# Performance work log

Hardware: AMD Instinct MI355X
Metric: run time of the kernel (lower is better)

The kernel has to match this reference:

```python
import jax, jax.numpy as jnp
import numpy as np
import math

H, N, L_DEFAULT = 1024, 64, 2048
DT_MIN, DT_MAX = 0.001, 0.1
EPS = 1e-7


def hippo_skew_evals(n):
    # eigenvalues of (Hippo - Hippo.T)/2, sorted by descending imaginary part
    i = np.arange(n, dtype=np.float64)
    x = 2.0 * i + 1.0
    hippo = np.sqrt(np.outer(x, x)) * np.tri(n, n, -1)  # strictly lower triangular
    skew = (hippo - hippo.T) / 2.0
    evals = np.linalg.eigvals(skew)
    return evals[np.argsort(-evals.imag)]


def setup_inputs() -> dict:
    rng = np.random.default_rng(0)
    # Lambda init: hippo_skew_pos_imag -> w = evals(2N)[:N] - 0.5 (real part -0.5 < 0)
    w = hippo_skew_evals(2 * N)[:N] - 0.5
    Lambda_log_neg_re = np.log(-w.real).astype(np.float32)  # (N,)
    Lambda_im = w.imag.astype(np.float32)                   # (N,)
    # log_dt ~ U[log dt_min, log dt_max], tiled to (H,2) since sep_dt_re_im=True
    log_dt = (math.log(DT_MIN) + rng.random(H) * (math.log(DT_MAX) - math.log(DT_MIN))).astype(np.float32)
    log_dt = np.tile(log_dt[:, None], (1, 2))               # (H,2)
    W = rng.standard_normal((H, N, 2)).astype(np.float32)   # real view of complex (H,N)
    return {
        'log_dt': jnp.asarray(log_dt),
        'Lambda_log_neg_re': jnp.asarray(Lambda_log_neg_re),
        'Lambda_im': jnpp if False else jnp.asarray(Lambda_im),
        'W': jnp.asarray(W),
        'L': L_DEFAULT,
    }


def _reciprocal_clamped(x, eps=EPS):
    # conj(x) / max(|x|^2, eps^2)  -- matches DSS reciprocal(..., clamp=True)
    norm_sq = jnp.maximum((x * jnp.conj(x)).real, eps * eps)
    return jnp.conj(x) / norm_sq


def reference(log_dt, Lambda_log_neg_re, Lambda_im, W, L):
    Lam = -jnp.exp(Lambda_log_neg_re) + 1j * Lambda_im              # (N,) complex
    Wc = W[..., 0] + 1j * W[..., 1]                                 # (H,N) complex
    dt = jnp.exp(log_dt)                                            # (H,2)
    # sep_dt_re_im: separate step sizes for real and imaginary parts
    dt_Lambda = dt[:, 0:1] * Lam.real + 1j * (dt[:, 1:2] * Lam.imag)  # (H,N) complex
    pos = jnp.arange(L, dtype=log_dt.dtype)                          # (L,)
    S = jnp.exp(dt_Lambda[None, :, :] * pos[:, None, None])          # (L,H,N) complex
    Wk = Wc * (jnp.exp(dt_Lambda) - 1.0) * _reciprocal_clamped(Lam)  # (H,N)
    # kernel: real part of sum_n W[h,n] * S[l,h,n]
    return jnp.einsum('hn,lhn->lh', Wk, S).real.astype(jnp.float32)  # (L,H)
```

## Files before the change

kernel.cpp:

```cpp
#include <hip/hip_runtime.h>
#include <math.h>

#define H_DIM 1024
#define N_DIM 64

typedef __attribute__((ext_vector_type(8))) _Float16 f16x8;
typedef __attribute__((ext_vector_type(4))) float f32x4;

__device__ __forceinline__ float2 cmul(float2 a, float2 b) {
    return make_float2(fmaf(a.x, b.x, -(a.y * b.y)),
                       fmaf(a.x, b.y,   a.y * b.x));
}

__device__ __forceinline__ unsigned pkh(float x, float y) {
    union { _Float16 h[2]; unsigned u; } p;
    p.h[0] = (_Float16)x; p.h[1] = (_Float16)y;
    return p.u;
}


__global__ __launch_bounds__(256, 4) void dss_mfma2(
    const float* __restrict__ log_dt,
    const float* __restrict__ llnr,
    const float* __restrict__ limv,
    const float* __restrict__ W,
    const int*   __restrict__ Lp,
    float* __restrict__ out)
{
    __shared__ unsigned lds_raw[4 * 2 * 16 * 68];

    const int tid  = threadIdx.x;
    const int w    = tid >> 6;
    const int lane = tid & 63;

    int htile, g;
    if (gridDim.y == 8 && gridDim.x == 128) {
        const int id = blockIdx.x + (blockIdx.y << 7);
        g = id & 7;
        const int q = id >> 3;
        htile = 4 * (q & 31) + (q >> 5);
    } else { htile = blockIdx.x; g = blockIdx.y; }

    const int h0 = htile * 8;
    const int L  = *Lp;
    const int fr = lane & 15;
    const int kg = lane >> 4;

    const float lre = -__expf(llnr[lane]);
    const float lmi = limv[lane];
    const float den = fmaxf(fmaf(lre, lre, lmi * lmi), 1e-14f);
    const float rde = __builtin_amdgcn_rcpf(den);
    const float rr = lre * rde, ri = -lmi * rde;

    unsigned* Atab = lds_raw + w * (2 * 16 * 68);
    unsigned* Btab = Atab + 16 * 68;

    f32x4 accs[2];

    #pragma unroll
    for (int j = 0; j < 2; ++j) {
        const int h = h0 + 2 * w + j;
        const float dt0 = __expf(log_dt[2 * h]);
        const float dt1 = __expf(log_dt[2 * h + 1]);
        const float a = dt0 * lre;
        const float b = dt1 * lmi;
        const float eA = __expf(a);
        const float sb = __sinf(b), cbv = __cosf(b);
        const float2 s = make_float2(eA * cbv, eA * sb);

        const float2 wc = ((const float2*)W)[(size_t)h * N_DIM + lane];
        const float2 em1 = make_float2(s.x - 1.0f, s.y);
        const float2 t  = make_float2(em1.x * rr - em1.y * ri,
                                      em1.x * ri + em1.y * rr);
        const float2 wk = make_float2(wc.x * t.x - wc.y * t.y,
                                      wc.x * t.y + wc.y * t.x);

        const float2 s2 = cmul(s, s), s4 = cmul(s2, s2), s8 = cmul(s4, s4);
        const float2 s12 = cmul(s8, s4), s16 = cmul(s8, s8);
        const float2 s32 = cmul(s16, s16), s64 = cmul(s32, s32);
        const float2 s128 = cmul(s64, s64), s192 = cmul(s128, s64);
        const float2 s256 = cmul(s128, s128);
        const float2 s512 = cmul(s256, s256), s1024 = cmul(s512, s512);

        float2 w0 = wk;
        if (g & 1) w0 = cmul(w0, s256);
        if (g & 2) w0 = cmul(w0, s512);
        if (g & 4) w0 = cmul(w0, s1024);

        float2 Bv[16];
        Bv[0] = make_float2(1.0f, 0.0f); Bv[4] = s4; Bv[8] = s8; Bv[12] = s12;
        #pragma unroll
        for (int k = 1; k < 4; ++k) {
            Bv[k]      = cmul(Bv[k - 1], s);
            Bv[4 + k]  = cmul(Bv[4 + k - 1], s);
            Bv[8 + k]  = cmul(Bv[8 + k - 1], s);
            Bv[12 + k] = cmul(Bv[12 + k - 1], s);
        }
        float2 Av[16];
        Av[0] = w0; Av[4] = cmul(w0, s64); Av[8] = cmul(w0, s128); Av[12] = cmul(w0, s192);
        #pragma unroll
        for (int k = 1; k < 4; ++k) {
            Av[k]      = cmul(Av[k - 1], s16);
            Av[4 + k]  = cmul(Av[4 + k - 1], s16);
            Av[8 + k]  = cmul(Av[8 + k - 1], s16);
            Av[12 + k] = cmul(Av[12 + k - 1], s16);
        }

        #pragma unroll
        for (int q = 0; q < 16; ++q)
            Atab[q * 68 + lane] = pkh(Av[q].x, Av[q].y);
        #pragma unroll
        for (int r = 0; r < 16; ++r)
            Btab[r * 68 + lane] = pkh(Bv[r].x, -Bv[r].y);

        f32x4 acc = {0.0f, 0.0f, 0.0f, 0.0f};
        #pragma unroll
        for (int c = 0; c < 4; ++c) {
            const f16x8 af = *(const f16x8*)&Atab[fr * 68 + 16 * c + 4 * kg];
            const f16x8 bf = *(const f16x8*)&Btab[fr * 68 + 16 * c + 4 * kg];
            acc = __builtin_amdgcn_mfma_f32_16x16x32_f16(af, bf, acc, 0, 0, 0);
        }
        accs[j] = acc;
    }

    __syncthreads();
    float* scr = (float*)lds_raw;
    #pragma unroll
    for (int j = 0; j < 2; ++j) {
        const int hl = 2 * w + j;
        #pragma unroll
        for (int reg = 0; reg < 4; ++reg)
            scr[(64 * kg + 16 * reg + fr) * 12 + hl] = accs[j][reg];
    }
    __syncthreads();

    const float4* scr4 = (const float4*)scr;
    float4* out4 = (float4*)out;
    const int l0 = g * 256;
    #pragma unroll
    for (int i = 0; i < 2; ++i) {
        const int flat = i * 256 + tid;
        const int l = flat >> 1, q = flat & 1;
        const int gl = l0 + l;
        if (gl < L)
            out4[(size_t)gl * (H_DIM / 4) + htile * 2 + q] = scr4[l * 3 + q];
    }
}


#define HT 64
#define CHUNK 16

__global__ __launch_bounds__(256) void dss_kernel_fb(
    const float* __restrict__ log_dt,
    const float* __restrict__ lam_log_neg_re,
    const float* __restrict__ lam_im,
    const float* __restrict__ W,
    const int*   __restrict__ Lp,
    float* __restrict__ out,
    int H, int N)
{
    __shared__ float4 params[N_DIM * HT];
    const int tid = threadIdx.x;
    const int h0 = blockIdx.x * HT;
    const int l0_blk = blockIdx.y * 64;
    const int L = *Lp;
    const float2* __restrict__ W2 = (const float2*)W;

    for (int flat = tid; flat < N * HT; flat += 256) {
        const int hl = flat & (HT - 1);
        const int n  = flat >> 6;
        const int h  = h0 + hl;
        const float dt0 = expf(log_dt[2 * h]);
        const float dt1 = expf(log_dt[2 * h + 1]);
        const float lre = -expf(lam_log_neg_re[n]);
        const float lmi = lam_im[n];
        const float a = dt0 * lre;
        const float b = dt1 * lmi;
        const float eA = expf(a);
        float sb, cb;
        sincosf(b, &sb, &cb);
        const float em1r = eA * cb - 1.0f;
        const float em1i = eA * sb;
        const float den = fmaxf(lre * lre + lmi * lmi, 1e-14f);
        const float rr =  lre / den;
        const float ri = -lmi / den;
        const float2 wc = W2[h * N + n];
        const float trm = em1r * rr - em1i * ri;
        const float tim = em1r * ri + em1i * rr;
        params[flat] = make_float4(a, b,
                                   wc.x * trm - wc.y * tim,
                                   wc.x * tim + wc.y * trm);
    }
    __syncthreads();

    const int hl = tid & (HT - 1);
    const int chunk = tid >> 6;
    const int l0 = l0_blk + chunk * CHUNK;
    if (l0 >= L) return;

    float acc[CHUNK];
    #pragma unroll
    for (int k = 0; k < CHUNK; ++k) acc[k] = 0.0f;

    const double TWO_PI  = 6.283185307179586476925286766559;
    const double INV_2PI = 0.15915494309189533576888376337251;

    for (int n = 0; n < N; ++n) {
        const float4 pp = params[n * HT + hl];
        const float a = pp.x, b = pp.y, wr = pp.z, wi = pp.w;
        double ph = (double)b * (double)l0;
        ph -= TWO_PI * rint(ph * INV_2PI);
        const float th = (float)ph;
        const float e0 = expf(a * (float)l0);
        float s0, c0;
        sincosf(th, &s0, &c0);
        float zr = e0 * c0;
        float zi = e0 * s0;
        const float eA = expf(a);
        float sb, cb;
        sincosf(b, &sb, &cb);
        const float str = eA * cb;
        const float sti = eA * sb;
        #pragma unroll
        for (int k = 0; k < CHUNK; ++k) {
            acc[k] = fmaf(wr, zr, fmaf(-wi, zi, acc[k]));
            const float nzr = zr * str - zi * sti;
            const float nzi = fmaf(zr, sti, zi * str);
            zr = nzr; zi = nzi;
        }
    }

    #pragma unroll
    for (int k = 0; k < CHUNK; ++k) {
        const int l = l0 + k;
        if (l < L) out[(size_t)l * H + h0 + hl] = acc[k];
    }
}


extern "C" void kernel_launch(void* const* d_in, const int* in_sizes, int n_in,
                              void* d_out, int out_size, void* d_ws, size_t ws_size,
                              hipStream_t stream) {
    const float* log_dt = (const float*)d_in[0];
    const float* llnr   = (const float*)d_in[1];
    const float* lim    = (const float*)d_in[2];
    const float* W      = (const float*)d_in[3];
    const int*   Lp     = (const int*)d_in[4];

    const int H = in_sizes[0] / 2;
    const int N = in_sizes[1];
    const int L = out_size / (H > 0 ? H : 1);

    if (H == H_DIM && N == N_DIM && L <= 2048) {
        dim3 grid(H_DIM / 8, (L + 255) / 256);
        dss_mfma2<<<grid, 256, 0, stream>>>(log_dt, llnr, lim, W, Lp, (float*)d_out);
    } else {
        dim3 grid((H + HT - 1) / HT, (L + 63) / 64);
        dss_kernel_fb<<<grid, 256, 0, stream>>>(log_dt, llnr, lim, W, Lp,
                                                (float*)d_out, H, N);
    }
}
```

Measured before the change: 13.05 us.

## Switch to 32x32x16 MFMA with one channel per wave and XOR-swizzled LDS

Replaces the 16x16x32 MFMA tiles with 32x32x16 MFMA. Each wave now produces a 32x32 block of positions (1024 L values) for one channel, using a 32-row A table of w·s^(32k) and a 32-row B table of s^k, and the grid becomes 256 h-tiles × 2 L-halves. LDS rows lose their padding and use an XOR swizzle to avoid bank conflicts, and output is written as one float4 per position across 4 channels. The intent is fewer blocks, less duplicated per-channel setup (exp, sin, power chains), and higher MFMA efficiency. In exchange, occupancy drops (launch bounds 2), register pressure rises with 16-wide accumulators, and the longer fp16 power chains may lose precision.

```diff
diff --git a/kernel.cpp b/kernel.cpp
--- a/kernel.cpp
+++ b/kernel.cpp
@@ -5,7 +5,7 @@
 #define N_DIM 64
 
 typedef __attribute__((ext_vector_type(8))) _Float16 f16x8;
-typedef __attribute__((ext_vector_type(4))) float f32x4;
+typedef __attribute__((ext_vector_type(16))) float f32x16;
 
 __device__ __forceinline__ float2 cmul(float2 a, float2 b) {
     return make_float2(fmaf(a.x, b.x, -(a.y * b.y)),
@@ -19,7 +19,7 @@
 }
 
 
-__global__ __launch_bounds__(256, 4) void dss_mfma2(
+__global__ __launch_bounds__(256, 2) void dss_mfma32(
     const float* __restrict__ log_dt,
     const float* __restrict__ llnr,
     const float* __restrict__ limv,
@@ -27,24 +27,29 @@
     const int*   __restrict__ Lp,
     float* __restrict__ out)
 {
-    __shared__ unsigned lds_raw[4 * 2 * 16 * 68];
+    __shared__ unsigned lds_raw[4 * 2 * 32 * 64];
 
     const int tid  = threadIdx.x;
     const int w    = tid >> 6;
     const int lane = tid & 63;
 
-    int htile, g;
-    if (gridDim.y == 8 && gridDim.x == 128) {
-        const int id = blockIdx.x + (blockIdx.y << 7);
-        g = id & 7;
-        const int q = id >> 3;
-        htile = 4 * (q & 31) + (q >> 5);
-    } else { htile = blockIdx.x; g = blockIdx.y; }
-
-    const int h0 = htile * 8;
+    const int raw = blockIdx.x + (blockIdx.y << 8);
+    const int r7 = raw & 7, q9 = raw >> 3;
+    const int half  = q9 >> 5;
+    const int htile = (r7 << 5) | (q9 & 31);
+
     const int L  = *Lp;
-    const int fr = lane & 15;
-    const int kg = lane >> 4;
+    const int l0 = half << 10;
+    if (l0 >= L) return;
+
+    const int h = htile * 4 + w;
+
+    unsigned* Atab = lds_raw + w * (2 * 32 * 64);
+    unsigned* Btab = Atab + 32 * 64;
+
+    int lx[8];
+    #pragma unroll
+    for (int m = 0; m < 8; ++m) lx[m] = lane ^ (m << 2);
 
     const float lre = -__expf(llnr[lane]);
     const float lmi = limv[lane];
@@ -52,98 +57,98 @@
     const float rde = __builtin_amdgcn_rcpf(den);
     const float rr = lre * rde, ri = -lmi * rde;
 
-    unsigned* Atab = lds_raw + w * (2 * 16 * 68);
-    unsigned* Btab = Atab + 16 * 68;
-
-    f32x4 accs[2];
-
-    #pragma unroll
-    for (int j = 0; j < 2; ++j) {
-        const int h = h0 + 2 * w + j;
-        const float dt0 = __expf(log_dt[2 * h]);
-        const float dt1 = __expf(log_dt[2 * h + 1]);
-        const float a = dt0 * lre;
-        const float b = dt1 * lmi;
-        const float eA = __expf(a);
-        const float sb = __sinf(b), cbv = __cosf(b);
-        const float2 s = make_float2(eA * cbv, eA * sb);
-
-        const float2 wc = ((const float2*)W)[(size_t)h * N_DIM + lane];
-        const float2 em1 = make_float2(s.x - 1.0f, s.y);
-        const float2 t  = make_float2(em1.x * rr - em1.y * ri,
-                                      em1.x * ri + em1.y * rr);
-        const float2 wk = make_float2(wc.x * t.x - wc.y * t.y,
-                                      wc.x * t.y + wc.y * t.x);
-
-        const float2 s2 = cmul(s, s), s4 = cmul(s2, s2), s8 = cmul(s4, s4);
-        const float2 s12 = cmul(s8, s4), s16 = cmul(s8, s8);
-        const float2 s32 = cmul(s16, s16), s64 = cmul(s32, s32);
-        const float2 s128 = cmul(s64, s64), s192 = cmul(s128, s64);
-        const float2 s256 = cmul(s128, s128);
-        const float2 s512 = cmul(s256, s256), s1024 = cmul(s512, s512);
-
-        float2 w0 = wk;
-        if (g & 1) w0 = cmul(w0, s256);
-        if (g & 2) w0 = cmul(w0, s512);
-        if (g & 4) w0 = cmul(w0, s1024);
-
-        float2 Bv[16];
-        Bv[0] = make_float2(1.0f, 0.0f); Bv[4] = s4; Bv[8] = s8; Bv[12] = s12;
+    const float dt0 = __expf(log_dt[2 * h]);
+    const float dt1 = __expf(log_dt[2 * h + 1]);
+    const float a = dt0 * lre;
+    const float b = dt1 * lmi;
+    const float eA = __expf(a);
+    const float snb = __sinf(b), csb = __cosf(b);
+    const float2 s = make_float2(eA * csb, eA * snb);
+
+    const float2 wc = ((const float2*)W)[(size_t)h * N_DIM + lane];
+    const float2 em1 = make_float2(s.x - 1.0f, s.y);
+    const float2 t  = make_float2(em1.x * rr - em1.y * ri,
+                                  em1.x * ri + em1.y * rr);
+    const float2 wk = make_float2(wc.x * t.x - wc.y * t.y,
+                                  wc.x * t.y + wc.y * t.x);
+
+    const float2 s2 = cmul(s, s), s4 = cmul(s2, s2), s8 = cmul(s4, s4);
+    const float2 s16 = cmul(s8, s8), s24 = cmul(s16, s8);
+    const float2 s32 = cmul(s16, s16), s64 = cmul(s32, s32);
+    const float2 s128 = cmul(s64, s64), s256 = cmul(s128, s128);
+    const float2 s512 = cmul(s256, s256), s768 = cmul(s512, s256);
+    const float2 s1024 = cmul(s512, s512);
+
+    const float2 w0 = half ? cmul(wk, s1024) : wk;
+
+    {
+        float2 v0 = make_float2(1.0f, 0.0f), v1 = s8, v2 = s16, v3 = s24;
+        Btab[ 0 * 64 + lx[0]] = pkh(v0.x, -v0.y);
+        Btab[ 8 * 64 + lx[0]] = pkh(v1.x, -v1.y);
+        Btab[16 * 64 + lx[0]] = pkh(v2.x, -v2.y);
+        Btab[24 * 64 + lx[0]] = pkh(v3.x, -v3.y);
         #pragma unroll
-        for (int k = 1; k < 4; ++k) {
-            Bv[k]      = cmul(Bv[k - 1], s);
-            Bv[4 + k]  = cmul(Bv[4 + k - 1], s);
-            Bv[8 + k]  = cmul(Bv[8 + k - 1], s);
-            Bv[12 + k] = cmul(Bv[12 + k - 1], s);
-        }
-        float2 Av[16];
-        Av[0] = w0; Av[4] = cmul(w0, s64); Av[8] = cmul(w0, s128); Av[12] = cmul(w0, s192);
+        for (int k = 1; k < 8; ++k) {
+            v0 = cmul(v0, s); v1 = cmul(v1, s);
+            v2 = cmul(v2, s); v3 = cmul(v3, s);
+            Btab[( 0 + k) * 64 + lx[k]] = pkh(v0.x, -v0.y);
+            Btab[( 8 + k) * 64 + lx[k]] = pkh(v1.x, -v1.y);
+            Btab[(16 + k) * 64 + lx[k]] = pkh(v2.x, -v2.y);
+            Btab[(24 + k) * 64 + lx[k]] = pkh(v3.x, -v3.y);
+        }
+    }
+    {
+        float2 v0 = w0, v1 = cmul(w0, s256), v2 = cmul(w0, s512), v3 = cmul(w0, s768);
+        Atab[ 0 * 64 + lx[0]] = pkh(v0.x, v0.y);
+        Atab[ 8 * 64 + lx[0]] = pkh(v1.x, v1.y);
+        Atab[16 * 64 + lx[0]] = pkh(v2.x, v2.y);
+        Atab[24 * 64 + lx[0]] = pkh(v3.x, v3.y);
         #pragma unroll
-        for (int k = 1; k < 4; ++k) {
-            Av[k]      = cmul(Av[k - 1], s16);
-            Av[4 + k]  = cmul(Av[4 + k - 1], s16);
-            Av[8 + k]  = cmul(Av[8 + k - 1], s16);
-            Av[12 + k] = cmul(Av[12 + k - 1], s16);
-        }
-
-        #pragma unroll
-        for (int q = 0; q < 16; ++q)
-            Atab[q * 68 + lane] = pkh(Av[q].x, Av[q].y);
-        #pragma unroll
-        for (int r = 0; r < 16; ++r)
-            Btab[r * 68 + lane] = pkh(Bv[r].x, -Bv[r].y);
-
-        f32x4 acc = {0.0f, 0.0f, 0.0f, 0.0f};
-        #pragma unroll
-        for (int c = 0; c < 4; ++c) {
-            const f16x8 af = *(const f16x8*)&Atab[fr * 68 + 16 * c + 4 * kg];
-            const f16x8 bf = *(const f16x8*)&Btab[fr * 68 + 16 * c + 4 * kg];
-            acc = __builtin_amdgcn_mfma_f32_16x16x32_f16(af, bf, acc, 0, 0, 0);
-        }
-        accs[j] = acc;
+        for (int k = 1; k < 8; ++k) {
+            v0 = cmul(v0, s32); v1 = cmul(v1, s32);
+            v2 = cmul(v2, s32); v3 = cmul(v3, s32);
+            Atab[( 0 + k) * 64 + lx[k]] = pkh(v0.x, v0.y);
+            Atab[( 8 + k) * 64 + lx[k]] = pkh(v1.x, v1.y);
+            Atab[(16 + k) * 64 + lx[k]] = pkh(v2.x, v2.y);
+            Atab[(24 + k) * 64 + lx[k]] = pkh(v3.x, v3.y);
+        }
+    }
+
+    const int row = lane & 31;
+    const int hi  = lane >> 5;
+    const unsigned rsw = (unsigned)((row & 7) << 2);
+    const unsigned* Arow = Atab + row * 64;
+    const unsigned* Brow = Btab + row * 64;
+    f32x16 acc = {0.0f, 0.0f, 0.0f, 0.0f, 0.0f, 0.0f, 0.0f, 0.0f,
+                  0.0f, 0.0f, 0.0f, 0.0f, 0.0f, 0.0f, 0.0f, 0.0f};
+    #pragma unroll
+    for (int c = 0; c < 8; ++c) {
+        const unsigned off = (unsigned)(8 * c + 4 * hi) ^ rsw;
+        const f16x8 af = *(const f16x8*)&Arow[off];
+        const f16x8 bf = *(const f16x8*)&Brow[off];
+        acc = __builtin_amdgcn_mfma_f32_32x32x16_f16(af, bf, acc, 0, 0, 0);
     }
 
     __syncthreads();
     float* scr = (float*)lds_raw;
-    #pragma unroll
-    for (int j = 0; j < 2; ++j) {
-        const int hl = 2 * w + j;
-        #pragma unroll
-        for (int reg = 0; reg < 4; ++reg)
-            scr[(64 * kg + 16 * reg + fr) * 12 + hl] = accs[j][reg];
+    const int r32 = lane & 31;
+    #pragma unroll
+    for (int reg = 0; reg < 16; ++reg) {
+        const int q = (reg & 3) + 8 * (reg >> 2) + 4 * hi;
+        scr[(32 * q + r32) * 5 + w] = acc[reg];
     }
     __syncthreads();
 
-    const float4* scr4 = (const float4*)scr;
     float4* out4 = (float4*)out;
-    const int l0 = g * 256;
-    #pragma unroll
-    for (int i = 0; i < 2; ++i) {
-        const int flat = i * 256 + tid;
-        const int l = flat >> 1, q = flat & 1;
+    #pragma unroll
+    for (int i = 0; i < 4; ++i) {
+        const int l = i * 256 + tid;
         const int gl = l0 + l;
-        if (gl < L)
-            out4[(size_t)gl * (H_DIM / 4) + htile * 2 + q] = scr4[l * 3 + q];
+        if (gl < L) {
+            const float* p = &scr[l * 5];
+            out4[(size_t)gl * (H_DIM / 4) + htile] =
+                make_float4(p[0], p[1], p[2], p[3]);
+        }
     }
 }
 
@@ -253,8 +258,9 @@
     const int L = out_size / (H > 0 ? H : 1);
 
     if (H == H_DIM && N == N_DIM && L <= 2048) {
-        dim3 grid(H_DIM / 8, (L + 255) / 256);
-        dss_mfma2<<<grid, 256, 0, stream>>>(log_dt, llnr, lim, W, Lp, (float*)d_out);
+        const int halves = (L + 1023) / 1024;
+        dim3 grid(H_DIM / 4, halves);
+        dss_mfma32<<<grid, 256, 0, stream>>>(log_dt, llnr, lim, W, Lp, (float*)d_out);
     } else {
         dim3 grid((H + HT - 1) / HT, (L + 63) / 64);
         dss_kernel_fb<<<grid, 256, 0, stream>>>(log_dt, llnr, lim, W, Lp,
```

After: 12.07 us. 1.08x faster.
